# Optimization experiments

Measured on AMD Instinct MI355X. Metric: run time of the kernel, lower is better.

Reference implementation:

```python
import jax, jax.numpy as jnp
import numpy as np

N_NODES = 50000


def setup_inputs() -> dict:
    key = jax.random.key(0)
    k1, k2, k3, k4 = jax.random.split(key, 4)
    N, E, D_IN, D_OUT = N_NODES, 1_600_000, 128, 128
    x = jax.random.normal(k1, (N, D_IN), dtype=jnp.float32)
    edge_index = jax.random.randint(k2, (2, E), 0, N, dtype=jnp.int64)
    W = jax.random.normal(k3, (D_IN, D_OUT), dtype=jnp.float32) * (1.0 / np.sqrt(D_IN))
    b = jax.random.normal(k4, (D_OUT,), dtype=jnp.float32) * 0.01
    return {"x": x, "edge_index": edge_index, "W": W, "b": b}


def reference(x, edge_index, W, b):
    N = x.shape[0]
    # add self loops: edge (i, i) for every node
    loops = jnp.arange(N, dtype=edge_index.dtype)
    row = jnp.concatenate([edge_index[0], loops])  # [E+N]
    col = jnp.concatenate([edge_index[1], loops])  # [E+N]
    # degree over col (matches torch_geometric degree(col, N))
    deg = jax.ops.segment_sum(jnp.ones_like(col, dtype=x.dtype), col, num_segments=N)
    deg_inv_sqrt = jnp.where(deg > 0, jax.lax.rsqrt(jnp.maximum(deg, 1.0)), 0.0)
    norm = deg_inv_sqrt[row] * deg_inv_sqrt[col]  # [E+N]
    # linear transform then gather-multiply-scatter (segment sum over row)
    xl = x @ W + b  # [N, D_OUT]
    msg = norm[:, None] * xl[col]  # [E+N, D_OUT]
    out = jax.ops.segment_sum(msg, row, num_segments=N)
    return out
```

## Files before the change

kernel.cpp:

```cpp
#include <hip/hip_runtime.h>
#include <hip/hip_bf16.h>


#define D     128
#define TILE  4096
#define BINB  1024
#define RPB   256
#define MAXB  256
#define SPLIT_CAP 16384

typedef short  bf16x8 __attribute__((ext_vector_type(8)));
typedef float  f32x4  __attribute__((ext_vector_type(4)));
typedef unsigned short us4 __attribute__((ext_vector_type(4)));
typedef unsigned short us8 __attribute__((ext_vector_type(8)));

static __device__ __forceinline__ unsigned short f2bf(float f) {
    unsigned u = __float_as_uint(f);
    u = (u + 0x7FFFu + ((u >> 16) & 1u)) >> 16;
    return (unsigned short)u;
}
static __device__ __forceinline__ float bf2f(unsigned short s) {
    return __uint_as_float(((unsigned)s) << 16);
}

__global__ __launch_bounds__(256) void k_prep(const float* __restrict__ W,
                                              unsigned short* __restrict__ wtb,
                                              int* __restrict__ bcur,
                                              int* __restrict__ bcurC,
                                              int NB, int CAP, int CAPC) {
    int i = blockIdx.x * 256 + threadIdx.x;
    if (i < NB) { bcur[i] = i * CAP; bcurC[i] = i * CAPC; }
    if (i < D * D) {
        int n = i >> 7, k = i & 127;
        wtb[n * 128 + k] = f2bf(W[k * 128 + n]);
    }
}

__global__ __launch_bounds__(BINB) void k_bin(const int* __restrict__ rows,
                                              const int* __restrict__ cols,
                                              int* __restrict__ bcur,
                                              int* __restrict__ bcurC,
                                              unsigned* __restrict__ ebuf,
                                              unsigned char* __restrict__ cebuf,
                                              int E, int NB, int CAP, int CAPC) {
    __shared__ unsigned sorted[TILE];
    __shared__ unsigned short sortedC[TILE];
    __shared__ int lcnt[MAXB], lbase[MAXB], excl[MAXB], cur[MAXB];
    __shared__ int lcntC[MAXB], lbaseC[MAXB], exclC[MAXB], curC[MAXB];
    const int t = threadIdx.x;
    const int base = blockIdx.x * TILE;
    int m = E - base; if (m > TILE) m = TILE;

    unsigned p[TILE / BINB];
    unsigned short q[TILE / BINB];
    #pragma unroll
    for (int it = 0; it < TILE / BINB; ++it) {
        int i = it * BINB + t;
        if (i < m) {
            unsigned r = (unsigned)rows[base + i];
            unsigned c = (unsigned)cols[base + i];
            p[it] = c | ((r & 255u) << 16) | ((r >> 8) << 24);
            q[it] = (unsigned short)c;
        }
    }
    for (int b = t; b < MAXB; b += BINB) { lcnt[b] = 0; lcntC[b] = 0; }
    __syncthreads();
    #pragma unroll
    for (int it = 0; it < TILE / BINB; ++it) {
        int i = it * BINB + t;
        if (i < m) {
            atomicAdd(&lcnt[p[it] >> 24], 1);
            atomicAdd(&lcntC[q[it] >> 8], 1);
        }
    }
    __syncthreads();
    if (t < 64) {
        int b4 = t * 4;
        int v0 = lcnt[b4], v1 = lcnt[b4+1], v2 = lcnt[b4+2], v3 = lcnt[b4+3];
        int s = v0+v1+v2+v3, inc = s;
        #pragma unroll
        for (int off = 1; off < 64; off <<= 1) { int o = __shfl_up(inc, off); if (t >= off) inc += o; }
        int ex = inc - s;
        excl[b4] = ex;          cur[b4]   = ex;
        excl[b4+1] = ex+v0;     cur[b4+1] = ex+v0;
        excl[b4+2] = ex+v0+v1;  cur[b4+2] = ex+v0+v1;
        excl[b4+3] = ex+v0+v1+v2; cur[b4+3] = ex+v0+v1+v2;
    } else if (t < 128) {
        int l = t - 64, b4 = l * 4;
        int v0 = lcntC[b4], v1 = lcntC[b4+1], v2 = lcntC[b4+2], v3 = lcntC[b4+3];
        int s = v0+v1+v2+v3, inc = s;
        #pragma unroll
        for (int off = 1; off < 64; off <<= 1) { int o = __shfl_up(inc, off); if (l >= off) inc += o; }
        int ex = inc - s;
        exclC[b4] = ex;           curC[b4]   = ex;
        exclC[b4+1] = ex+v0;      curC[b4+1] = ex+v0;
        exclC[b4+2] = ex+v0+v1;   curC[b4+2] = ex+v0+v1;
        exclC[b4+3] = ex+v0+v1+v2; curC[b4+3] = ex+v0+v1+v2;
    }
    for (int b = t; b < NB; b += BINB) {
        int c = lcnt[b];
        lbase[b] = c ? atomicAdd(&bcur[b], c) : 0;
        int cc = lcntC[b];
        lbaseC[b] = cc ? atomicAdd(&bcurC[b], cc) : 0;
    }
    __syncthreads();
    #pragma unroll
    for (int it = 0; it < TILE / BINB; ++it) {
        int i = it * BINB + t;
        if (i < m) {
            int pos  = atomicAdd(&cur[p[it] >> 24], 1);
            sorted[pos] = p[it];
            int posC = atomicAdd(&curC[q[it] >> 8], 1);
            sortedC[posC] = q[it];
        }
    }
    __syncthreads();
    #pragma unroll
    for (int it = 0; it < TILE / BINB; ++it) {
        int i = it * BINB + t;
        if (i < m) {
            unsigned pp = sorted[i];
            int bk = pp >> 24;
            int g  = lbase[bk] + i - excl[bk];
            if (g < (bk + 1) * CAP) ebuf[g] = pp & 0xFFFFFFu;
            unsigned short qq = sortedC[i];
            int bc = qq >> 8;
            int gc = lbaseC[bc] + i - exclC[bc];
            if (gc < (bc + 1) * CAPC) cebuf[gc] = (unsigned char)(qq & 255u);
        }
    }
}

__global__ __launch_bounds__(1024) void k_split(const int* __restrict__ bcur,
                                                const int* __restrict__ bcurC,
                                                const unsigned* __restrict__ ebuf,
                                                const unsigned char* __restrict__ cebuf,
                                                unsigned short* __restrict__ ecol,
                                                int* __restrict__ begN,
                                                int* __restrict__ endN,
                                                float* __restrict__ dis,
                                                int N, int CAP, int CAPC) {
    __shared__ unsigned short sorted[SPLIT_CAP];
    __shared__ int cnt[RPB];
    __shared__ int excl[RPB];
    __shared__ int cur[RPB];
    __shared__ int cntD[RPB];
    const int b = blockIdx.x, t = threadIdx.x;
    const int base = b * CAP;
    int m = bcur[b] - base; if (m > CAP) m = CAP;
    const int baseC = b * CAPC;
    int mD = bcurC[b] - baseC; if (mD > CAPC) mD = CAPC;
    if (t < RPB) { cnt[t] = 0; cntD[t] = 0; }
    __syncthreads();
    const unsigned* cw = (const unsigned*)(cebuf + baseC);
    int nw = mD >> 2;
    for (int i = t; i < nw; i += 1024) {
        unsigned u = cw[i];
        atomicAdd(&cntD[u & 255u], 1);
        atomicAdd(&cntD[(u >> 8) & 255u], 1);
        atomicAdd(&cntD[(u >> 16) & 255u], 1);
        atomicAdd(&cntD[u >> 24], 1);
    }
    if (t < (mD & 3)) atomicAdd(&cntD[cebuf[baseC + nw * 4 + t]], 1);
    for (int i = t; i < m; i += 1024)
        atomicAdd(&cnt[(ebuf[base + i] >> 16) & 255], 1);
    __syncthreads();
    const int row0 = b * RPB;
    if (t < RPB && row0 + t < N)
        dis[row0 + t] = rsqrtf((float)(cntD[t] + 1));
    if (t < 64) {
        int b4 = t * 4;
        int v0 = cnt[b4], v1 = cnt[b4+1], v2 = cnt[b4+2], v3 = cnt[b4+3];
        int s = v0+v1+v2+v3, inc = s;
        #pragma unroll
        for (int off = 1; off < 64; off <<= 1) { int o = __shfl_up(inc, off); if (t >= off) inc += o; }
        int ex = inc - s;
        excl[b4] = ex;            cur[b4]   = ex;
        excl[b4+1] = ex+v0;       cur[b4+1] = ex+v0;
        excl[b4+2] = ex+v0+v1;    cur[b4+2] = ex+v0+v1;
        excl[b4+3] = ex+v0+v1+v2; cur[b4+3] = ex+v0+v1+v2;
    }
    __syncthreads();
    if (t < RPB && row0 + t < N) {
        begN[row0 + t] = base + excl[t];
        endN[row0 + t] = base + excl[t] + cnt[t];
    }
    for (int i = t; i < m; i += 1024) {
        unsigned p = ebuf[base + i];
        int pos = atomicAdd(&cur[(p >> 16) & 255], 1);
        sorted[pos] = (unsigned short)(p & 0xFFFFu);
    }
    __syncthreads();
    for (int i = t; i < m; i += 1024)
        ecol[base + i] = sorted[i];
}

__global__ __launch_bounds__(256) void k_gemm(const float* __restrict__ x,
                                              const unsigned short* __restrict__ wtb,
                                              const float* __restrict__ bia,
                                              unsigned short* __restrict__ xlb,
                                              int N) {
    __shared__ unsigned short wt[128][136];
    __shared__ unsigned short xs[64][136];
    const int t = threadIdx.x;
    const int row0 = blockIdx.x * 64;

    #pragma unroll
    for (int i = 0; i < 8; ++i) {
        int j = i * 256 + t;
        int n = j >> 4, k8 = j & 15;
        us8 v = *(const us8*)&wtb[j * 8];
        *(us8*)&wt[n][k8 * 8] = v;
    }
    #pragma unroll
    for (int i = 0; i < 8; ++i) {
        int j = i * 256 + t;
        int r = j >> 5, c4 = j & 31;
        int gr = row0 + r;
        us4 o = (us4){0, 0, 0, 0};
        if (gr < N) {
            float4 v = *(const float4*)&x[(size_t)gr * D + c4 * 4];
            o = (us4){f2bf(v.x), f2bf(v.y), f2bf(v.z), f2bf(v.w)};
        }
        *(us4*)&xs[r][c4 * 4] = o;
    }
    __syncthreads();

    const int w  = t >> 6, l = t & 63;
    const int m0 = w * 16;
    const int lm = l & 15, lq = l >> 4;

    f32x4 acc[8];
    #pragma unroll
    for (int nt = 0; nt < 8; ++nt) acc[nt] = (f32x4){0.f, 0.f, 0.f, 0.f};

    #pragma unroll
    for (int kk = 0; kk < 4; ++kk) {
        const int kof = kk * 32 + lq * 8;
        bf16x8 a = *(const bf16x8*)&xs[m0 + lm][kof];
        #pragma unroll
        for (int nt = 0; nt < 8; ++nt) {
            bf16x8 bb = *(const bf16x8*)&wt[nt * 16 + lm][kof];
            acc[nt] = __builtin_amdgcn_mfma_f32_16x16x32_bf16(a, bb, acc[nt], 0, 0, 0);
        }
    }

    #pragma unroll
    for (int nt = 0; nt < 8; ++nt) {
        const int col = nt * 16 + lm;
        const float bc = bia[col];
        #pragma unroll
        for (int r = 0; r < 4; ++r) {
            int grow = row0 + m0 + lq * 4 + r;
            if (grow < N) xlb[(size_t)grow * D + col] = f2bf(acc[nt][r] + bc);
        }
    }
}

__global__ __launch_bounds__(256) void k_reduce(const int* __restrict__ begN,
                                                const int* __restrict__ endN,
                                                const unsigned short* __restrict__ ecol,
                                                const float* __restrict__ dis,
                                                const unsigned short* __restrict__ xlb,
                                                float* __restrict__ out, int N) {
    const int wave = threadIdx.x >> 6;
    const int lane = threadIdx.x & 63;
    const int i = blockIdx.x * 4 + wave;
    if (i >= N) return;
    const float di = dis[i];

    const ushort2 sv = *reinterpret_cast<const ushort2*>(xlb + (size_t)i * D + lane * 2);
    float ax = di * di * bf2f(sv.x);
    float ay = di * di * bf2f(sv.y);

    const int beg = begN[i], end = endN[i];
    for (int base = beg; base < end; base += 64) {
        int m = end - base; if (m > 64) m = 64;
        int   c = 0;
        float n = 0.0f;
        if (lane < m) {
            c = ecol[base + lane];
            n = di * dis[c];
        }
        for (int j = 0; j < m; j += 8) {
            float vx[8], vy[8], nn[8];
            #pragma unroll
            for (int u = 0; u < 8; ++u) {
                int cc = __shfl(c, j + u);
                ushort2 s = *reinterpret_cast<const ushort2*>(xlb + (size_t)cc * D + lane * 2);
                vx[u] = bf2f(s.x);
                vy[u] = bf2f(s.y);
                nn[u] = __shfl(n, j + u);
            }
            #pragma unroll
            for (int u = 0; u < 8; ++u) {
                ax = fmaf(nn[u], vx[u], ax);
                ay = fmaf(nn[u], vy[u], ay);
            }
        }
    }
    *reinterpret_cast<float2*>(out + (size_t)i * D + lane * 2) = make_float2(ax, ay);
}

__global__ __launch_bounds__(256) void k_zero(int* __restrict__ p, int n) {
    int i = blockIdx.x * 256 + threadIdx.x;
    if (i < n) p[i] = 0;
}
__global__ __launch_bounds__(256) void k_deg(const int* __restrict__ cols,
                                             int* __restrict__ cntc, int E) {
    int e = blockIdx.x * 256 + threadIdx.x;
    if (e < E) atomicAdd(&cntc[cols[e]], 1);
}
__global__ __launch_bounds__(256) void k_dis(const int* __restrict__ cntc,
                                             float* __restrict__ dis, int N) {
    int i = blockIdx.x * 256 + threadIdx.x;
    if (i < N) dis[i] = rsqrtf((float)(cntc[i] + 1));
}
#define GEMM_R 8
__global__ __launch_bounds__(128) void k_gemmf(const float* __restrict__ x,
                                               const float* __restrict__ W,
                                               const float* __restrict__ b,
                                               float* __restrict__ xl, int N) {
    __shared__ float xs[GEMM_R][D];
    const int c  = threadIdx.x;
    const int r0 = blockIdx.x * GEMM_R;
    #pragma unroll
    for (int r = 0; r < GEMM_R; ++r) {
        int row = r0 + r;
        xs[r][c] = (row < N) ? x[row * D + c] : 0.0f;
    }
    __syncthreads();
    float acc[GEMM_R];
    const float bc = b[c];
    #pragma unroll
    for (int r = 0; r < GEMM_R; ++r) acc[r] = bc;
    for (int k = 0; k < D; k += 4) {
        const float w0 = W[(k + 0) * D + c];
        const float w1 = W[(k + 1) * D + c];
        const float w2 = W[(k + 2) * D + c];
        const float w3 = W[(k + 3) * D + c];
        #pragma unroll
        for (int r = 0; r < GEMM_R; ++r) {
            const float4 xv = *reinterpret_cast<const float4*>(&xs[r][k]);
            acc[r] = fmaf(xv.x, w0, acc[r]);
            acc[r] = fmaf(xv.y, w1, acc[r]);
            acc[r] = fmaf(xv.z, w2, acc[r]);
            acc[r] = fmaf(xv.w, w3, acc[r]);
        }
    }
    #pragma unroll
    for (int r = 0; r < GEMM_R; ++r) {
        int row = r0 + r;
        if (row < N) xl[row * D + c] = acc[r];
    }
}
__global__ __launch_bounds__(256) void k_self(const float* __restrict__ xl,
                                              const float* __restrict__ dis,
                                              float* __restrict__ out, int N) {
    int gid = blockIdx.x * 256 + threadIdx.x;
    int i = gid >> 7;
    if (i < N) {
        float d = dis[i];
        out[gid] = d * d * xl[gid];
    }
}
__global__ __launch_bounds__(256) void k_scatter(const int* __restrict__ rows,
                                                 const int* __restrict__ cols,
                                                 const float* __restrict__ dis,
                                                 const float* __restrict__ xl,
                                                 float* __restrict__ out, int E) {
    long long gid = (long long)blockIdx.x * 256 + threadIdx.x;
    int e    = (int)(gid >> 6);
    int lane = (int)(gid & 63);
    if (e >= E) return;
    const int row = rows[e];
    const int col = cols[e];
    const float nrm = dis[row] * dis[col];
    atomicAdd(&out[row * D + lane],      nrm * xl[col * D + lane]);
    atomicAdd(&out[row * D + 64 + lane], nrm * xl[col * D + 64 + lane]);
}

extern "C" void kernel_launch(void* const* d_in, const int* in_sizes, int n_in,
                              void* d_out, int out_size, void* d_ws, size_t ws_size,
                              hipStream_t stream) {
    const float* x   = (const float*)d_in[0];
    const int*   ei  = (const int*)d_in[1];
    const float* W   = (const float*)d_in[2];
    const float* b   = (const float*)d_in[3];
    float*       out = (float*)d_out;

    const int N = in_sizes[0] / D;
    const int E = in_sizes[1] / 2;
    const int* rows = ei;
    const int* cols = ei + E;
    const int NB = (N + RPB - 1) / RPB;
    const int NT = (E + TILE - 1) / TILE;
    const int CAP  = (((2 * E) / NB) + 63) / 64 * 64;
    const int CAPC = CAP;

    char* p = (char*)d_ws;
    size_t off = 0;
    unsigned short* xlb   = (unsigned short*)(p + off); off += (size_t)N * D * 2;
    unsigned short* wtb   = (unsigned short*)(p + off); off += (size_t)D * D * 2;
    float*          dis   = (float*)(p + off);          off += (size_t)N * 4;
    int*            bcur  = (int*)(p + off);            off += (size_t)MAXB * 4;
    int*            bcurC = (int*)(p + off);            off += (size_t)MAXB * 4;
    int*            begN  = (int*)(p + off);            off += (size_t)N * 4;
    int*            endN  = (int*)(p + off);            off += (size_t)N * 4;
    unsigned*       ebuf  = (unsigned*)(p + off);       off += (size_t)NB * CAP * 4;
    unsigned short* ecol  = (unsigned short*)(p + off); off += (size_t)NB * CAP * 2;
    unsigned char*  cebuf = (unsigned char*)(p + off);  off += (size_t)NB * CAPC;

    const int gN = (N + 255) / 256;
    const int gE = (E + 255) / 256;

    if (N <= 65536 && NB <= MAXB && CAP <= SPLIT_CAP && ws_size >= off) {
        k_prep  <<<(D * D + 255) / 256, 256, 0, stream>>>(W, wtb, bcur, bcurC, NB, CAP, CAPC);
        k_bin   <<<NT, BINB, 0, stream>>>(rows, cols, bcur, bcurC, ebuf, cebuf, E, NB, CAP, CAPC);
        k_split <<<NB, 1024, 0, stream>>>(bcur, bcurC, ebuf, cebuf, ecol, begN, endN, dis, N, CAP, CAPC);
        k_gemm  <<<(N + 63) / 64, 256, 0, stream>>>(x, wtb, b, xlb, N);
        k_reduce<<<(N + 3) / 4, 256, 0, stream>>>(begN, endN, ecol, dis, xlb, out, N);
    } else {
        char* q = (char*)d_ws;
        float* xl   = (float*)q;
        float* disF = (float*)(q + (size_t)N * D * 4);
        int*   cc   = (int*)(q + (size_t)N * D * 4 + (size_t)N * 4);
        k_zero <<<gN, 256, 0, stream>>>(cc, N);
        k_deg  <<<gE, 256, 0, stream>>>(cols, cc, E);
        k_dis  <<<gN, 256, 0, stream>>>(cc, disF, N);
        k_gemmf<<<(N + GEMM_R - 1) / GEMM_R, 128, 0, stream>>>(x, W, b, xl, N);
        k_self <<<((N * D) + 255) / 256, 256, 0, stream>>>(xl, disF, out, N);
        long long st = (long long)E * 64;
        k_scatter<<<(int)((st + 255) / 256), 256, 0, stream>>>(rows, cols, disF, xl, out, E);
    }
}
```

Measured before the change: 173.3 us.

## Fuse GEMM into binning kernel as extra blocks and shrink row buckets

The bf16 MFMA GEMM blocks are merged into the edge-binning launch as extra blocks, so the transform runs alongside binning instead of in its own launch. Rows per bucket drop from 256 to 128 (up to 512 buckets) and the binning tile doubles to 8192 edges, which raises split-kernel parallelism and halves its shared-memory sort size. In exchange the GEMM blocks run at 1024 threads with only 256 active and a 64KB static shared buffer, which can lower occupancy, and with finer buckets each binning tile issues more global atomics.

```diff
diff --git a/kernel.cpp b/kernel.cpp
--- a/kernel.cpp
+++ b/kernel.cpp
@@ -3,11 +3,11 @@
 
 
 #define D     128
-#define TILE  4096
+#define TILE  8192
 #define BINB  1024
-#define RPB   256
-#define MAXB  256
-#define SPLIT_CAP 16384
+#define RPB   128
+#define MAXB  512
+#define SPLIT_CAP 8192
 
 typedef short  bf16x8 __attribute__((ext_vector_type(8)));
 typedef float  f32x4  __attribute__((ext_vector_type(4)));
@@ -36,18 +36,82 @@
     }
 }
 
-__global__ __launch_bounds__(BINB) void k_bin(const int* __restrict__ rows,
-                                              const int* __restrict__ cols,
-                                              int* __restrict__ bcur,
-                                              int* __restrict__ bcurC,
-                                              unsigned* __restrict__ ebuf,
-                                              unsigned char* __restrict__ cebuf,
-                                              int E, int NB, int CAP, int CAPC) {
-    __shared__ unsigned sorted[TILE];
-    __shared__ unsigned short sortedC[TILE];
-    __shared__ int lcnt[MAXB], lbase[MAXB], excl[MAXB], cur[MAXB];
-    __shared__ int lcntC[MAXB], lbaseC[MAXB], exclC[MAXB], curC[MAXB];
+__global__ __launch_bounds__(1024) void k_binjoint(
+        const int* __restrict__ rows, const int* __restrict__ cols,
+        int* __restrict__ bcur, int* __restrict__ bcurC,
+        unsigned* __restrict__ ebuf, unsigned char* __restrict__ cebuf,
+        const float* __restrict__ x, const unsigned short* __restrict__ wtb,
+        const float* __restrict__ bia, unsigned short* __restrict__ xlb,
+        int E, int N, int NB, int CAP, int CAPC, int NT) {
+    __shared__ __align__(16) unsigned char smem[65536];
     const int t = threadIdx.x;
+
+    if ((int)blockIdx.x >= NT) {
+        unsigned short (*wt)[136] = (unsigned short (*)[136])smem;
+        unsigned short (*xs)[136] = (unsigned short (*)[136])(smem + 34816);
+        const int row0 = ((int)blockIdx.x - NT) * 64;
+        #pragma unroll
+        for (int i = 0; i < 2; ++i) {
+            int j = i * 1024 + t;
+            int n = j >> 4, k8 = j & 15;
+            us8 v = *(const us8*)&wtb[j * 8];
+            *(us8*)&wt[n][k8 * 8] = v;
+        }
+        #pragma unroll
+        for (int i = 0; i < 2; ++i) {
+            int j = i * 1024 + t;
+            int r = j >> 5, c4 = j & 31;
+            int gr = row0 + r;
+            us4 o = (us4){0, 0, 0, 0};
+            if (gr < N) {
+                float4 v = *(const float4*)&x[(size_t)gr * D + c4 * 4];
+                o = (us4){f2bf(v.x), f2bf(v.y), f2bf(v.z), f2bf(v.w)};
+            }
+            *(us4*)&xs[r][c4 * 4] = o;
+        }
+        __syncthreads();
+        if (t < 256) {
+            const int w  = t >> 6, l = t & 63;
+            const int m0 = w * 16;
+            const int lm = l & 15, lq = l >> 4;
+            f32x4 acc[8];
+            #pragma unroll
+            for (int nt = 0; nt < 8; ++nt) acc[nt] = (f32x4){0.f, 0.f, 0.f, 0.f};
+            #pragma unroll
+            for (int kk = 0; kk < 4; ++kk) {
+                const int kof = kk * 32 + lq * 8;
+                bf16x8 a = *(const bf16x8*)&xs[m0 + lm][kof];
+                #pragma unroll
+                for (int nt = 0; nt < 8; ++nt) {
+                    bf16x8 bb = *(const bf16x8*)&wt[nt * 16 + lm][kof];
+                    acc[nt] = __builtin_amdgcn_mfma_f32_16x16x32_bf16(a, bb, acc[nt], 0, 0, 0);
+                }
+            }
+            #pragma unroll
+            for (int nt = 0; nt < 8; ++nt) {
+                const int col = nt * 16 + lm;
+                const float bc = bia[col];
+                #pragma unroll
+                for (int r = 0; r < 4; ++r) {
+                    int grow = row0 + m0 + lq * 4 + r;
+                    if (grow < N) xlb[(size_t)grow * D + col] = f2bf(acc[nt][r] + bc);
+                }
+            }
+        }
+        return;
+    }
+
+    unsigned*       sorted  = (unsigned*)smem;
+    unsigned short* sortedC = (unsigned short*)(smem + 32768);
+    int* lcnt   = (int*)(smem + 49152);
+    int* lbase  = lcnt + 512;
+    int* excl   = lcnt + 1024;
+    int* cur    = lcnt + 1536;
+    int* lcntC  = lcnt + 2048;
+    int* lbaseC = lcnt + 2560;
+    int* exclC  = lcnt + 3072;
+    int* curC   = lcnt + 3584;
+
     const int base = blockIdx.x * TILE;
     int m = E - base; if (m > TILE) m = TILE;
 
@@ -59,43 +123,41 @@
         if (i < m) {
             unsigned r = (unsigned)rows[base + i];
             unsigned c = (unsigned)cols[base + i];
-            p[it] = c | ((r & 255u) << 16) | ((r >> 8) << 24);
+            p[it] = c | ((r & 127u) << 16) | ((r >> 7) << 23);
             q[it] = (unsigned short)c;
         }
     }
-    for (int b = t; b < MAXB; b += BINB) { lcnt[b] = 0; lcntC[b] = 0; }
+    if (t < 512) { lcnt[t] = 0; lcntC[t] = 0; }
     __syncthreads();
     #pragma unroll
     for (int it = 0; it < TILE / BINB; ++it) {
         int i = it * BINB + t;
         if (i < m) {
-            atomicAdd(&lcnt[p[it] >> 24], 1);
-            atomicAdd(&lcntC[q[it] >> 8], 1);
+            atomicAdd(&lcnt[p[it] >> 23], 1);
+            atomicAdd(&lcntC[q[it] >> 7], 1);
         }
     }
     __syncthreads();
     if (t < 64) {
-        int b4 = t * 4;
-        int v0 = lcnt[b4], v1 = lcnt[b4+1], v2 = lcnt[b4+2], v3 = lcnt[b4+3];
-        int s = v0+v1+v2+v3, inc = s;
+        int k0 = t * 8, v[8], s = 0;
+        #pragma unroll
+        for (int u = 0; u < 8; ++u) { v[u] = lcnt[k0 + u]; s += v[u]; }
+        int inc = s;
         #pragma unroll
         for (int off = 1; off < 64; off <<= 1) { int o = __shfl_up(inc, off); if (t >= off) inc += o; }
-        int ex = inc - s;
-        excl[b4] = ex;          cur[b4]   = ex;
-        excl[b4+1] = ex+v0;     cur[b4+1] = ex+v0;
-        excl[b4+2] = ex+v0+v1;  cur[b4+2] = ex+v0+v1;
-        excl[b4+3] = ex+v0+v1+v2; cur[b4+3] = ex+v0+v1+v2;
+        int run = inc - s;
+        #pragma unroll
+        for (int u = 0; u < 8; ++u) { excl[k0 + u] = run; cur[k0 + u] = run; run += v[u]; }
     } else if (t < 128) {
-        int l = t - 64, b4 = l * 4;
-        int v0 = lcntC[b4], v1 = lcntC[b4+1], v2 = lcntC[b4+2], v3 = lcntC[b4+3];
-        int s = v0+v1+v2+v3, inc = s;
+        int l = t - 64, k0 = l * 8, v[8], s = 0;
+        #pragma unroll
+        for (int u = 0; u < 8; ++u) { v[u] = lcntC[k0 + u]; s += v[u]; }
+        int inc = s;
         #pragma unroll
         for (int off = 1; off < 64; off <<= 1) { int o = __shfl_up(inc, off); if (l >= off) inc += o; }
-        int ex = inc - s;
-        exclC[b4] = ex;           curC[b4]   = ex;
-        exclC[b4+1] = ex+v0;      curC[b4+1] = ex+v0;
-        exclC[b4+2] = ex+v0+v1;   curC[b4+2] = ex+v0+v1;
-        exclC[b4+3] = ex+v0+v1+v2; curC[b4+3] = ex+v0+v1+v2;
+        int run = inc - s;
+        #pragma unroll
+        for (int u = 0; u < 8; ++u) { exclC[k0 + u] = run; curC[k0 + u] = run; run += v[u]; }
     }
     for (int b = t; b < NB; b += BINB) {
         int c = lcnt[b];
@@ -108,9 +170,9 @@
     for (int it = 0; it < TILE / BINB; ++it) {
         int i = it * BINB + t;
         if (i < m) {
-            int pos  = atomicAdd(&cur[p[it] >> 24], 1);
+            int pos  = atomicAdd(&cur[p[it] >> 23], 1);
             sorted[pos] = p[it];
-            int posC = atomicAdd(&curC[q[it] >> 8], 1);
+            int posC = atomicAdd(&curC[q[it] >> 7], 1);
             sortedC[posC] = q[it];
         }
     }
@@ -120,13 +182,13 @@
         int i = it * BINB + t;
         if (i < m) {
             unsigned pp = sorted[i];
-            int bk = pp >> 24;
+            int bk = pp >> 23;
             int g  = lbase[bk] + i - excl[bk];
-            if (g < (bk + 1) * CAP) ebuf[g] = pp & 0xFFFFFFu;
+            if (g < (bk + 1) * CAP) ebuf[g] = pp & 0x7FFFFFu;
             unsigned short qq = sortedC[i];
-            int bc = qq >> 8;
+            int bc = qq >> 7;
             int gc = lbaseC[bc] + i - exclC[bc];
-            if (gc < (bc + 1) * CAPC) cebuf[gc] = (unsigned char)(qq & 255u);
+            if (gc < (bc + 1) * CAPC) cebuf[gc] = (unsigned char)(qq & 127u);
         }
     }
 }
@@ -163,22 +225,19 @@
     }
     if (t < (mD & 3)) atomicAdd(&cntD[cebuf[baseC + nw * 4 + t]], 1);
     for (int i = t; i < m; i += 1024)
-        atomicAdd(&cnt[(ebuf[base + i] >> 16) & 255], 1);
+        atomicAdd(&cnt[(ebuf[base + i] >> 16) & 127], 1);
     __syncthreads();
     const int row0 = b * RPB;
     if (t < RPB && row0 + t < N)
         dis[row0 + t] = rsqrtf((float)(cntD[t] + 1));
     if (t < 64) {
-        int b4 = t * 4;
-        int v0 = cnt[b4], v1 = cnt[b4+1], v2 = cnt[b4+2], v3 = cnt[b4+3];
-        int s = v0+v1+v2+v3, inc = s;
+        int v0 = cnt[2 * t], v1 = cnt[2 * t + 1];
+        int s = v0 + v1, inc = s;
         #pragma unroll
         for (int off = 1; off < 64; off <<= 1) { int o = __shfl_up(inc, off); if (t >= off) inc += o; }
         int ex = inc - s;
-        excl[b4] = ex;            cur[b4]   = ex;
-        excl[b4+1] = ex+v0;       cur[b4+1] = ex+v0;
-        excl[b4+2] = ex+v0+v1;    cur[b4+2] = ex+v0+v1;
-        excl[b4+3] = ex+v0+v1+v2; cur[b4+3] = ex+v0+v1+v2;
+        excl[2 * t] = ex;          cur[2 * t] = ex;
+        excl[2 * t + 1] = ex + v0; cur[2 * t + 1] = ex + v0;
     }
     __syncthreads();
     if (t < RPB && row0 + t < N) {
@@ -187,74 +246,12 @@
     }
     for (int i = t; i < m; i += 1024) {
         unsigned p = ebuf[base + i];
-        int pos = atomicAdd(&cur[(p >> 16) & 255], 1);
+        int pos = atomicAdd(&cur[(p >> 16) & 127], 1);
         sorted[pos] = (unsigned short)(p & 0xFFFFu);
     }
     __syncthreads();
     for (int i = t; i < m; i += 1024)
         ecol[base + i] = sorted[i];
-}
-
-__global__ __launch_bounds__(256) void k_gemm(const float* __restrict__ x,
-                                              const unsigned short* __restrict__ wtb,
-                                              const float* __restrict__ bia,
-                                              unsigned short* __restrict__ xlb,
-                                              int N) {
-    __shared__ unsigned short wt[128][136];
-    __shared__ unsigned short xs[64][136];
-    const int t = threadIdx.x;
-    const int row0 = blockIdx.x * 64;
-
-    #pragma unroll
-    for (int i = 0; i < 8; ++i) {
-        int j = i * 256 + t;
-        int n = j >> 4, k8 = j & 15;
-        us8 v = *(const us8*)&wtb[j * 8];
-        *(us8*)&wt[n][k8 * 8] = v;
-    }
-    #pragma unroll
-    for (int i = 0; i < 8; ++i) {
-        int j = i * 256 + t;
-        int r = j >> 5, c4 = j & 31;
-        int gr = row0 + r;
-        us4 o = (us4){0, 0, 0, 0};
-        if (gr < N) {
-            float4 v = *(const float4*)&x[(size_t)gr * D + c4 * 4];
-            o = (us4){f2bf(v.x), f2bf(v.y), f2bf(v.z), f2bf(v.w)};
-        }
-        *(us4*)&xs[r][c4 * 4] = o;
-    }
-    __syncthreads();
-
-    const int w  = t >> 6, l = t & 63;
-    const int m0 = w * 16;
-    const int lm = l & 15, lq = l >> 4;
-
-    f32x4 acc[8];
-    #pragma unroll
-    for (int nt = 0; nt < 8; ++nt) acc[nt] = (f32x4){0.f, 0.f, 0.f, 0.f};
-
-    #pragma unroll
-    for (int kk = 0; kk < 4; ++kk) {
-        const int kof = kk * 32 + lq * 8;
-        bf16x8 a = *(const bf16x8*)&xs[m0 + lm][kof];
-        #pragma unroll
-        for (int nt = 0; nt < 8; ++nt) {
-            bf16x8 bb = *(const bf16x8*)&wt[nt * 16 + lm][kof];
-            acc[nt] = __builtin_amdgcn_mfma_f32_16x16x32_bf16(a, bb, acc[nt], 0, 0, 0);
-        }
-    }
-
-    #pragma unroll
-    for (int nt = 0; nt < 8; ++nt) {
-        const int col = nt * 16 + lm;
-        const float bc = bia[col];
-        #pragma unroll
-        for (int r = 0; r < 4; ++r) {
-            int grow = row0 + m0 + lq * 4 + r;
-            if (grow < N) xlb[(size_t)grow * D + col] = f2bf(acc[nt][r] + bc);
-        }
-    }
 }
 
 __global__ __launch_bounds__(256) void k_reduce(const int* __restrict__ begN,
@@ -395,6 +392,7 @@
     const int* cols = ei + E;
     const int NB = (N + RPB - 1) / RPB;
     const int NT = (E + TILE - 1) / TILE;
+    const int GN = (N + 63) / 64;
     const int CAP  = (((2 * E) / NB) + 63) / 64 * 64;
     const int CAPC = CAP;
 
@@ -415,11 +413,11 @@
     const int gE = (E + 255) / 256;
 
     if (N <= 65536 && NB <= MAXB && CAP <= SPLIT_CAP && ws_size >= off) {
-        k_prep  <<<(D * D + 255) / 256, 256, 0, stream>>>(W, wtb, bcur, bcurC, NB, CAP, CAPC);
-        k_bin   <<<NT, BINB, 0, stream>>>(rows, cols, bcur, bcurC, ebuf, cebuf, E, NB, CAP, CAPC);
-        k_split <<<NB, 1024, 0, stream>>>(bcur, bcurC, ebuf, cebuf, ecol, begN, endN, dis, N, CAP, CAPC);
-        k_gemm  <<<(N + 63) / 64, 256, 0, stream>>>(x, wtb, b, xlb, N);
-        k_reduce<<<(N + 3) / 4, 256, 0, stream>>>(begN, endN, ecol, dis, xlb, out, N);
+        k_prep    <<<(D * D + 255) / 256, 256, 0, stream>>>(W, wtb, bcur, bcurC, NB, CAP, CAPC);
+        k_binjoint<<<NT + GN, BINB, 0, stream>>>(rows, cols, bcur, bcurC, ebuf, cebuf,
+                                                 x, wtb, b, xlb, E, N, NB, CAP, CAPC, NT);
+        k_split   <<<NB, 1024, 0, stream>>>(bcur, bcurC, ebuf, cebuf, ecol, begN, endN, dis, N, CAP, CAPC);
+        k_reduce  <<<(N + 3) / 4, 256, 0, stream>>>(begN, endN, ecol, dis, xlb, out, N);
     } else {
         char* q = (char*)d_ws;
         float* xl   = (float*)q;
```

Result: faster. 161.1 us (-7.0%).
